# Optimization experiments

Measured on AMD Instinct MI355X. Metric: run time of the kernel, lower is better.

## Reference

```python
import jax, jax.numpy as jnp
import numpy as np

H_IMG, W_IMG, N_GAUSS = 256, 256, 512


def setup_inputs() -> dict:
    key = jax.random.key(0)
    k1, k2, k3, k4 = jax.random.split(key, 4)
    # Gaussian centers uniformly inside the image (pixel coords)
    means_2d = jax.random.uniform(k1, (N_GAUSS, 2), dtype=jnp.float32) * jnp.array([W_IMG, H_IMG], dtype=jnp.float32)
    # SPD 2x2 covariances: A A^T + eps*I, scaled to a few-pixel footprint
    A = jax.random.normal(k2, (N_GAUSS, 2, 2), dtype=jnp.float32) * 3.0
    cov_2d = jnp.einsum('nij,nkj->nik', A, A) + 0.3 * jnp.eye(2, dtype=jnp.float32)[None]
    opacities = jax.random.uniform(k3, (N_GAUSS,), dtype=jnp.float32)
    colors = jax.random.uniform(k4, (N_GAUSS, 3), dtype=jnp.float32)
    return {"means_2d": means_2d, "cov_2d": cov_2d, "opacities": opacities,
            "colors": colors, "H": H_IMG, "W": W_IMG}


def reference(means_2d, cov_2d, opacities, colors, H, W):
    # pixel centers [H, W, 2] in (x, y) order, +0.5 center offset
    gy, gx = jnp.meshgrid(jnp.arange(H), jnp.arange(W), indexing='ij')
    pix = jnp.stack([gx, gy], axis=-1).astype(jnp.float32) + 0.5

    # analytic 2x2 inverse of each covariance
    a, b = cov_2d[:, 0, 0], cov_2d[:, 0, 1]
    c, d = cov_2d[:, 1, 0], cov_2d[:, 1, 1]
    det = a * d - b * c
    inv_cov = jnp.stack([jnp.stack([d, -b], axis=-1),
                         jnp.stack([-c, a], axis=-1)], axis=-2) / det[:, None, None]  # [N,2,2]

    dx = pix[:, :, None, :] - means_2d[None, None, :, :]            # [H,W,N,2]
    intermediate = jnp.einsum('hwnk,nkl->hwnl', dx, inv_cov)        # [H,W,N,2]
    mahalanobis = jnp.sum(intermediate * dx, axis=-1)               # [H,W,N]
    gaussian_weight = jnp.exp(-0.5 * mahalanobis)

    alpha = opacities[None, None, :] * gaussian_weight              # [H,W,N]
    cumprod = jnp.cumprod(1.0 - alpha + 1e-7, axis=-1)
    transmittance = jnp.concatenate(
        [jnp.ones((H, W, 1), dtype=alpha.dtype), cumprod[:, :, :-1]], axis=-1)
    weights = alpha * transmittance
    rendered = jnp.einsum('hwn,nc->hwc', weights, colors)           # [H,W,3]
    return rendered
```

## Files before the change

kernel.cpp:

```cpp
#include <hip/hip_runtime.h>

#ifndef __has_builtin
#define __has_builtin(x) 0
#endif

__device__ __forceinline__ float fast_exp2(float x) {
#if __has_builtin(__builtin_amdgcn_exp2f)
  return __builtin_amdgcn_exp2f(x);
#else
  return exp2f(x);
#endif
}
__device__ __forceinline__ float fast_rcp(float x) {
#if __has_builtin(__builtin_amdgcn_rcpf)
  return __builtin_amdgcn_rcpf(x);
#else
  return 1.0f / x;
#endif
}

#define NG     512
#define NSEG   8
#define SEGLEN 64
#define PXB    128
#define QCUT   -21.0f

__global__ __launch_bounds__(512, 4) void render_kernel(
    const float* __restrict__ means, const float* __restrict__ cov,
    const float* __restrict__ opac,  const float* __restrict__ cols,
    float* __restrict__ out)
{
  __shared__ float4 arrA[NG];
  __shared__ float2 arrB[NG];
  __shared__ float4 colp[NG];
  __shared__ float4 rowp[NG];
  __shared__ float4 part[NSEG][PXB];
  __shared__ float  outstage[PXB * 3];

  const int tid = threadIdx.x;

  {
    const int g = tid;
    const float mx = means[2*g], my = means[2*g+1];
    const float a = cov[4*g+0], b = cov[4*g+1], c = cov[4*g+2], d = cov[4*g+3];
    const float inv = 1.0f / (a*d - b*c);
    const float HL2E = 0.72134752f;
    const float ka = -HL2E * d * inv;
    const float kb =  HL2E * (b + c) * inv;
    const float kc = -HL2E * a * inv;
    const float ko = log2f(opac[g]);
    arrA[g] = make_float4(mx, my, ka, kb);
    arrB[g] = make_float2(kc, ko);
    colp[g] = make_float4(cols[3*g+0], cols[3*g+1], cols[3*g+2], 0.f);
  }
  __syncthreads();

  const int lane = tid & 63;
  const int seg  = tid >> 6;
  const int pixbase = blockIdx.x * PXB;
  const float py  = (float)(pixbase >> 8) + 0.5f;
  const float x0f = (float)(pixbase & 255) + 0.5f;
  const float px0 = x0f + (float)lane;

  unsigned long long mask;
  {
    const int gt = seg * SEGLEN + lane;
    const float4 A  = arrA[gt];
    const float2 Bq = arrB[gt];
    const float dy = py - A.y;
    const float Bv = A.w * dy;
    const float cc = fmaf(Bq.x * dy, dy, Bq.y);
    rowp[gt] = make_float4(A.x, A.z, Bv, cc);
    const float lo = x0f - A.x;
    const float hi = lo + 127.0f;
    float dxs = Bv * (-0.5f * fast_rcp(A.z));
    dxs = fminf(fmaxf(dxs, lo), hi);
    const float q = fmaf(fmaf(A.z, dxs, Bv), dxs, cc);
    mask = __ballot(q > QCUT);
  }

  float T0 = 1.f, T1 = 1.f;
  float r0 = 0.f, g0 = 0.f, b0 = 0.f, r1 = 0.f, g1 = 0.f, b1 = 0.f;
  while (mask) {
    const int bit = __ffsll(mask) - 1;
    mask &= mask - 1;
    const int g = seg * SEGLEN + bit;
    const float4 P = rowp[g];
    const float4 C = colp[g];
    const float dx0 = px0 - P.x;
    const float dx1 = dx0 + 64.0f;
    const float m0 = fmaf(fmaf(P.y, dx0, P.z), dx0, P.w);
    const float m1 = fmaf(fmaf(P.y, dx1, P.z), dx1, P.w);
    const float a0 = fast_exp2(m0);
    const float a1 = fast_exp2(m1);
    const float aw0 = a0 * T0;
    const float aw1 = a1 * T1;
    r0 = fmaf(aw0, C.x, r0); g0 = fmaf(aw0, C.y, g0); b0 = fmaf(aw0, C.z, b0);
    r1 = fmaf(aw1, C.x, r1); g1 = fmaf(aw1, C.y, g1); b1 = fmaf(aw1, C.z, b1);
    T0 *= (1.0000001f - a0);
    T1 *= (1.0000001f - a1);
  }

  part[seg][lane]      = make_float4(r0, g0, b0, T0);
  part[seg][lane + 64] = make_float4(r1, g1, b1, T1);
  __syncthreads();

  if (tid < PXB) {
    float T = 1.f, R = 0.f, G = 0.f, B = 0.f;
#pragma unroll
    for (int s = 0; s < NSEG; ++s) {
      const float4 p = part[s][tid];
      R = fmaf(T, p.x, R);
      G = fmaf(T, p.y, G);
      B = fmaf(T, p.z, B);
      T *= p.w;
    }
    outstage[tid*3+0] = R;
    outstage[tid*3+1] = G;
    outstage[tid*3+2] = B;
  }
  __syncthreads();

  if (tid < PXB * 3) {
    out[pixbase * 3 + tid] = outstage[tid];
  }
}

extern "C" void kernel_launch(void* const* d_in, const int* in_sizes, int n_in,
                              void* d_out, int out_size, void* d_ws, size_t ws_size,
                              hipStream_t stream) {
  const float* means = (const float*)d_in[0];
  const float* cov   = (const float*)d_in[1];
  const float* opac  = (const float*)d_in[2];
  const float* cols  = (const float*)d_in[3];
  float* out = (float*)d_out;
  (void)in_sizes; (void)n_in; (void)out_size; (void)d_ws; (void)ws_size;
  render_kernel<<<dim3(256 * 256 / PXB), dim3(512), 0, stream>>>(
      means, cov, opac, cols, out);
}
```

Baseline: 65.42 us.

## Halve pixels per block and compact live Gaussians per segment

Each block now covers 64 pixels instead of 128, so each thread handles one pixel and the occupancy hint doubles. Each thread preprocesses its own Gaussian straight from global memory, which drops the separate shared-memory setup pass and one barrier. Live Gaussians are stream-compacted per wave via ballot and popcount into shared arrays, so the inner loop becomes a dense counted loop instead of bit scanning. This gives finer culling per 64-pixel row segment but doubles the number of blocks, so the per-block preprocessing is repeated more often. The final store relies on outstage being written and read within the same single wave (64 threads), using only a threadfence_block instead of a barrier.

```diff
diff --git a/kernel.cpp b/kernel.cpp
--- a/kernel.cpp
+++ b/kernel.cpp
@@ -22,39 +22,20 @@
 #define NG     512
 #define NSEG   8
 #define SEGLEN 64
-#define PXB    128
+#define PXB    64
 #define QCUT   -21.0f
 
-__global__ __launch_bounds__(512, 4) void render_kernel(
+__global__ __launch_bounds__(512, 8) void render_kernel(
     const float* __restrict__ means, const float* __restrict__ cov,
     const float* __restrict__ opac,  const float* __restrict__ cols,
     float* __restrict__ out)
 {
-  __shared__ float4 arrA[NG];
-  __shared__ float2 arrB[NG];
-  __shared__ float4 colp[NG];
-  __shared__ float4 rowp[NG];
+  __shared__ float4 srow[NSEG][SEGLEN];
+  __shared__ float4 scol[NSEG][SEGLEN];
   __shared__ float4 part[NSEG][PXB];
   __shared__ float  outstage[PXB * 3];
 
-  const int tid = threadIdx.x;
-
-  {
-    const int g = tid;
-    const float mx = means[2*g], my = means[2*g+1];
-    const float a = cov[4*g+0], b = cov[4*g+1], c = cov[4*g+2], d = cov[4*g+3];
-    const float inv = 1.0f / (a*d - b*c);
-    const float HL2E = 0.72134752f;
-    const float ka = -HL2E * d * inv;
-    const float kb =  HL2E * (b + c) * inv;
-    const float kc = -HL2E * a * inv;
-    const float ko = log2f(opac[g]);
-    arrA[g] = make_float4(mx, my, ka, kb);
-    arrB[g] = make_float2(kc, ko);
-    colp[g] = make_float4(cols[3*g+0], cols[3*g+1], cols[3*g+2], 0.f);
-  }
-  __syncthreads();
-
+  const int tid  = threadIdx.x;
   const int lane = tid & 63;
   const int seg  = tid >> 6;
   const int pixbase = blockIdx.x * PXB;
@@ -62,67 +43,72 @@
   const float x0f = (float)(pixbase & 255) + 0.5f;
   const float px0 = x0f + (float)lane;
 
-  unsigned long long mask;
+  int n;
   {
-    const int gt = seg * SEGLEN + lane;
-    const float4 A  = arrA[gt];
-    const float2 Bq = arrB[gt];
-    const float dy = py - A.y;
-    const float Bv = A.w * dy;
-    const float cc = fmaf(Bq.x * dy, dy, Bq.y);
-    rowp[gt] = make_float4(A.x, A.z, Bv, cc);
-    const float lo = x0f - A.x;
-    const float hi = lo + 127.0f;
-    float dxs = Bv * (-0.5f * fast_rcp(A.z));
+    const int g = seg * SEGLEN + lane;
+    const float2 mu = ((const float2*)means)[g];
+    const float4 cv = ((const float4*)cov)[g];
+    const float  op = opac[g];
+    const float  c0 = cols[3*g+0], c1 = cols[3*g+1], c2 = cols[3*g+2];
+    const float inv = fast_rcp(fmaf(cv.x, cv.w, -cv.y * cv.z));
+    const float HL2E = 0.72134752f;
+    const float ka = -HL2E * cv.w * inv;
+    const float kb =  HL2E * (cv.y + cv.z) * inv;
+    const float kc = -HL2E * cv.x * inv;
+    const float ko = log2f(op);
+    const float dy = py - mu.y;
+    const float Bv = kb * dy;
+    const float cc = fmaf(kc * dy, dy, ko);
+    const float lo = x0f - mu.x;
+    const float hi = lo + (float)(PXB - 1);
+    float dxs = Bv * (-0.5f * fast_rcp(ka));
     dxs = fminf(fmaxf(dxs, lo), hi);
-    const float q = fmaf(fmaf(A.z, dxs, Bv), dxs, cc);
-    mask = __ballot(q > QCUT);
+    const float q = fmaf(fmaf(ka, dxs, Bv), dxs, cc);
+    const bool live = (q > QCUT);
+    const unsigned long long mask = __ballot(live);
+    n = __popcll(mask);
+    if (live) {
+      const int ci = __popcll(mask & ((1ull << lane) - 1ull));
+      srow[seg][ci] = make_float4(mu.x, ka, Bv, cc);
+      scol[seg][ci] = make_float4(c0, c1, c2, 0.f);
+    }
   }
 
-  float T0 = 1.f, T1 = 1.f;
-  float r0 = 0.f, g0 = 0.f, b0 = 0.f, r1 = 0.f, g1 = 0.f, b1 = 0.f;
-  while (mask) {
-    const int bit = __ffsll(mask) - 1;
-    mask &= mask - 1;
-    const int g = seg * SEGLEN + bit;
-    const float4 P = rowp[g];
-    const float4 C = colp[g];
-    const float dx0 = px0 - P.x;
-    const float dx1 = dx0 + 64.0f;
-    const float m0 = fmaf(fmaf(P.y, dx0, P.z), dx0, P.w);
-    const float m1 = fmaf(fmaf(P.y, dx1, P.z), dx1, P.w);
-    const float a0 = fast_exp2(m0);
-    const float a1 = fast_exp2(m1);
-    const float aw0 = a0 * T0;
-    const float aw1 = a1 * T1;
-    r0 = fmaf(aw0, C.x, r0); g0 = fmaf(aw0, C.y, g0); b0 = fmaf(aw0, C.z, b0);
-    r1 = fmaf(aw1, C.x, r1); g1 = fmaf(aw1, C.y, g1); b1 = fmaf(aw1, C.z, b1);
-    T0 *= (1.0000001f - a0);
-    T1 *= (1.0000001f - a1);
+  float T = 1.f, R = 0.f, G = 0.f, B = 0.f;
+#pragma unroll 2
+  for (int i = 0; i < n; ++i) {
+    const float4 P = srow[seg][i];
+    const float4 C = scol[seg][i];
+    const float dx = px0 - P.x;
+    const float m  = fmaf(fmaf(P.y, dx, P.z), dx, P.w);
+    const float a  = fast_exp2(m);
+    const float aw = a * T;
+    R = fmaf(aw, C.x, R);
+    G = fmaf(aw, C.y, G);
+    B = fmaf(aw, C.z, B);
+    T *= (1.0000001f - a);
   }
 
-  part[seg][lane]      = make_float4(r0, g0, b0, T0);
-  part[seg][lane + 64] = make_float4(r1, g1, b1, T1);
+  part[seg][lane] = make_float4(R, G, B, T);
   __syncthreads();
 
   if (tid < PXB) {
-    float T = 1.f, R = 0.f, G = 0.f, B = 0.f;
+    float Tt = 1.f, Rr = 0.f, Gg = 0.f, Bb = 0.f;
 #pragma unroll
     for (int s = 0; s < NSEG; ++s) {
       const float4 p = part[s][tid];
-      R = fmaf(T, p.x, R);
-      G = fmaf(T, p.y, G);
-      B = fmaf(T, p.z, B);
-      T *= p.w;
+      Rr = fmaf(Tt, p.x, Rr);
+      Gg = fmaf(Tt, p.y, Gg);
+      Bb = fmaf(Tt, p.z, Bb);
+      Tt *= p.w;
     }
-    outstage[tid*3+0] = R;
-    outstage[tid*3+1] = G;
-    outstage[tid*3+2] = B;
-  }
-  __syncthreads();
-
-  if (tid < PXB * 3) {
-    out[pixbase * 3 + tid] = outstage[tid];
+    outstage[tid*3+0] = Rr;
+    outstage[tid*3+1] = Gg;
+    outstage[tid*3+2] = Bb;
+    __threadfence_block();
+    out[pixbase*3 +       tid] = outstage[      tid];
+    out[pixbase*3 +  64 + tid] = outstage[ 64 + tid];
+    out[pixbase*3 + 128 + tid] = outstage[128 + tid];
   }
 }
 
```

New measurement: 64.30 us. No clear change (-1.7%).
